# Kernel tuning notes

Hardware: AMD Instinct MI355X
Metric: run time of the kernel (lower is better)

## Reference

```python
import jax, jax.numpy as jnp
import numpy as np

ROPE_BASE = 10000.0

def _rope(x):
    # x: (B, T, H, hd); rotate-half RoPE
    B, T, H, hd = x.shape
    half = hd // 2
    inv_freq = 1.0 / (ROPE_BASE ** (jnp.arange(half, dtype=jnp.float32) / half))
    ang = jnp.arange(T, dtype=jnp.float32)[:, None] * inv_freq[None, :]  # (T, half)
    cos = jnp.cos(ang)[None, :, None, :]
    sin = jnp.sin(ang)[None, :, None, :]
    x1, x2 = x[..., :half], x[..., half:]
    return jnp.concatenate([x1 * cos - x2 * sin, x1 * sin + x2 * cos], axis=-1)

def setup_inputs() -> dict:
    key = jax.random.key(0)
    k1, k2, k3 = jax.random.split(key, 3)
    B, T, D = 4, 2048, 2048
    x = jax.random.normal(k1, (B, T, D), dtype=jnp.float32)
    attn_mask = jnp.ones((B, T), dtype=bool)
    w_qkv = jax.random.normal(k2, (3 * D, D), dtype=jnp.float32) * (D ** -0.5)
    w_out = jax.random.normal(k3, (D, D), dtype=jnp.float32) * (D ** -0.5)
    return {"x": x, "attn_mask": attn_mask, "is_causal": 1, "w_qkv": w_qkv, "w_out": w_out}

def reference(x, attn_mask, is_causal, w_qkv, w_out):
    B, T, D = x.shape
    H = 16
    hd = D // H
    qkv = jnp.einsum('btd,ed->bte', x, w_qkv)  # (B, T, 3D)
    q, k, v = jnp.split(qkv, 3, axis=2)
    q = _rope(q.reshape(B, T, H, hd))
    k = _rope(k.reshape(B, T, H, hd))
    v = v.reshape(B, T, H, hd)
    scale = 1.0 / jnp.sqrt(jnp.float32(hd))
    scores = jnp.einsum('bqhd,bkhd->bhqk', q, k) * scale  # (B, H, T, T)
    if is_causal:
        mask = jnp.tril(jnp.ones((T, T), dtype=bool))[None, None]
    else:
        mask = attn_mask[:, None, None, :]  # (B,1,1,T)
    scores = jnp.where(mask, scores, jnp.finfo(scores.dtype).min)
    attn = jax.nn.softmax(scores, axis=-1)
    y = jnp.einsum('bhqk,bkhd->bqhd', attn, v).reshape(B, T, D)
    return jnp.einsum('btd,ed->bte', y, w_out)
```

## Files before the change

kernel.cpp:

```cpp
#include <hip/hip_runtime.h>
#include <stdint.h>
#include <stddef.h>

typedef float f32x4 __attribute__((ext_vector_type(4)));
typedef __bf16 bf16x8 __attribute__((ext_vector_type(8)));
typedef short s16x4 __attribute__((ext_vector_type(4)));

#define DEVI static __device__ __forceinline__

DEVI float bf2f(unsigned short u) {
  unsigned int x = ((unsigned int)u) << 16;
  float f;
  __builtin_memcpy(&f, &x, 4);
  return f;
}
DEVI unsigned short f2bf(float f) {
  unsigned int x;
  __builtin_memcpy(&x, &f, 4);
  unsigned int r = (x + 0x7fffu + ((x >> 16) & 1u)) >> 16;
  return (unsigned short)r;
}

DEVI void async16(const void* g, void* l) {
  __builtin_amdgcn_global_load_lds((__attribute__((address_space(1))) void*)g,
                                   (__attribute__((address_space(3))) void*)l,
                                   16, 0, 0);
}

#define BAR_LGKM()                                          \
  do {                                                      \
    asm volatile("s_waitcnt lgkmcnt(0)" ::: "memory");      \
    __builtin_amdgcn_s_barrier();                           \
    __builtin_amdgcn_sched_barrier(0);                      \
  } while (0)

#define BAR_VM(N)                                               \
  do {                                                          \
    asm volatile("s_waitcnt vmcnt(" #N ")" ::: "memory");       \
    __builtin_amdgcn_s_barrier();                               \
    __builtin_amdgcn_sched_barrier(0);                          \
  } while (0)

__global__ __launch_bounds__(256) void cvt_bf16(const float* __restrict__ in,
                                                unsigned short* __restrict__ out, int n) {
  int i = (blockIdx.x * 256 + threadIdx.x) * 4;
  if (i >= n) return;
  float4 v = *(const float4*)(in + i);
  s16x4 o;
  o[0] = (short)f2bf(v.x);
  o[1] = (short)f2bf(v.y);
  o[2] = (short)f2bf(v.z);
  o[3] = (short)f2bf(v.w);
  *(s16x4*)(out + i) = o;
}

__global__ __launch_bounds__(256) void rope_table(float* __restrict__ tab) {
  int idx = blockIdx.x * 256 + threadIdx.x;
  if (idx >= 2048 * 64) return;
  int tt = idx >> 6, j = idx & 63;
  float inv = powf(10000.0f, -(float)j * (1.0f / 64.0f));
  float ang = (float)tt * inv;
  tab[tt * 128 + j] = cosf(ang);
  tab[tt * 128 + 64 + j] = sinf(ang);
}

__global__ __launch_bounds__(256) void rope_apply(unsigned short* __restrict__ Qg,
                                                  unsigned short* __restrict__ Kg,
                                                  const float* __restrict__ tab) {
  const float S2 = 0.0883883476483184f * 1.44269504088896341f;
  int idx = blockIdx.x * 256 + threadIdx.x;
  int j4 = idx & 15;
  int tt = (idx >> 4) & 2047;
  int bh = idx >> 15;
  size_t base = ((size_t)bh * 2048 + tt) * 128;
  f32x4 c4 = *(const f32x4*)(tab + tt * 128 + j4 * 4);
  f32x4 s4 = *(const f32x4*)(tab + tt * 128 + 64 + j4 * 4);
  s16x4 q1 = *(const s16x4*)(Qg + base + j4 * 4);
  s16x4 q2 = *(const s16x4*)(Qg + base + 64 + j4 * 4);
  s16x4 k1 = *(const s16x4*)(Kg + base + j4 * 4);
  s16x4 k2 = *(const s16x4*)(Kg + base + 64 + j4 * 4);
  s16x4 o1, o2, p1, p2;
#pragma unroll
  for (int r = 0; r < 4; ++r) {
    float c = c4[r], s = s4[r];
    float a = bf2f((unsigned short)q1[r]), b2 = bf2f((unsigned short)q2[r]);
    o1[r] = (short)f2bf((a * c - b2 * s) * S2);
    o2[r] = (short)f2bf((a * s + b2 * c) * S2);
    float ka = bf2f((unsigned short)k1[r]), kb = bf2f((unsigned short)k2[r]);
    p1[r] = (short)f2bf(ka * c - kb * s);
    p2[r] = (short)f2bf(ka * s + kb * c);
  }
  *(s16x4*)(Qg + base + j4 * 4) = o1;
  *(s16x4*)(Qg + base + 64 + j4 * 4) = o2;
  *(s16x4*)(Kg + base + j4 * 4) = p1;
  *(s16x4*)(Kg + base + 64 + j4 * 4) = p2;
}

template <int EPI>
__global__ __launch_bounds__(512) void gemm256(const unsigned short* __restrict__ A,
                                               const unsigned short* __restrict__ B,
                                               float* __restrict__ C, int M, int N, int K,
                                               unsigned short* __restrict__ Q,
                                               unsigned short* __restrict__ Kk,
                                               unsigned short* __restrict__ VT) {
  __shared__ __attribute__((aligned(128))) unsigned short Al[2][2][8192];
  __shared__ __attribute__((aligned(128))) unsigned short Bl[2][2][8192];
  const int t = threadIdx.x;
  const int lane = t & 63;
  const int w = t >> 6, wr = w >> 2, wc = w & 3;
  const int g = lane >> 4, lr = lane & 15;

  const int id = blockIdx.y * gridDim.x + blockIdx.x;
  const int nwg = gridDim.x * gridDim.y;
  const int wg = (id & 7) * (nwg >> 3) + (id >> 3);
  const int bm = (wg / gridDim.x) * 256, bn = (wg % gridDim.x) * 256;

  const unsigned short* aptr = A + (size_t)bm * K;
  const unsigned short* bptr = B + (size_t)bn * K;

  const int srow = t >> 3;
  const int sslot = (t & 7) ^ (srow & 7);

#define STG(arr, mat, p, h, kt)                                                   \
  do {                                                                            \
    const unsigned short* _s =                                                    \
        (mat) + (size_t)((h) * 128 + srow) * K + (size_t)(kt) * 64 + sslot * 8;   \
    async16(_s, &arr[p][h][t * 8]);                                               \
    async16(_s + (size_t)64 * K, &arr[p][h][t * 8 + 4096]);                       \
  } while (0)

  const int u0 = ((g ^ (lr & 7)) * 8) + lr * 64;
  const int u1 = (((4 + g) ^ (lr & 7)) * 8) + lr * 64;

#define LDA_(p, mh)                                                               \
  _Pragma("unroll") for (int mf = 0; mf < 4; ++mf) {                              \
    af[mf][0] = *(const bf16x8*)&Al[p][wr][(mh) * 4096 + mf * 1024 + u0];         \
    af[mf][1] = *(const bf16x8*)&Al[p][wr][(mh) * 4096 + mf * 1024 + u1];         \
  }
#define LDB_(dst, p, nh)                                                          \
  _Pragma("unroll") for (int nf = 0; nf < 2; ++nf) {                              \
    dst[nf][0] = *(const bf16x8*)&Bl[p][wc >> 1][(wc & 1) * 4096 + (nh) * 2048 +  \
                                                 nf * 1024 + u0];                 \
    dst[nf][1] = *(const bf16x8*)&Bl[p][wc >> 1][(wc & 1) * 4096 + (nh) * 2048 +  \
                                                 nf * 1024 + u1];                 \
  }
#define MMA_(bsrc, mh, nh)                                                        \
  __builtin_amdgcn_s_setprio(1);                                                  \
  _Pragma("unroll") for (int mf = 0; mf < 4; ++mf)                                \
      _Pragma("unroll") for (int nf = 0; nf < 2; ++nf) {                          \
    acc[(mh) * 4 + mf][(nh) * 2 + nf] = __builtin_amdgcn_mfma_f32_16x16x32_bf16(  \
        af[mf][0], bsrc[nf][0], acc[(mh) * 4 + mf][(nh) * 2 + nf], 0, 0, 0);      \
    acc[(mh) * 4 + mf][(nh) * 2 + nf] = __builtin_amdgcn_mfma_f32_16x16x32_bf16(  \
        af[mf][1], bsrc[nf][1], acc[(mh) * 4 + mf][(nh) * 2 + nf], 0, 0, 0);      \
  }                                                                               \
  __builtin_amdgcn_s_setprio(0);
#define BARR() __builtin_amdgcn_s_barrier();

  f32x4 acc[8][4] = {};
  bf16x8 af[4][2], bfrA[2][2], bfrB[2][2];

  STG(Al, aptr, 0, 0, 0);
  STG(Al, aptr, 0, 1, 0);
  STG(Bl, bptr, 0, 0, 0);
  STG(Bl, bptr, 0, 1, 0);
  STG(Bl, bptr, 1, 0, 1);
  STG(Bl, bptr, 1, 1, 1);
  asm volatile("s_waitcnt vmcnt(4)" ::: "memory");
  __builtin_amdgcn_s_barrier();

  const int NITER = K >> 7;
  for (int i = 0; i < NITER; ++i) {
    const bool G = (i + 1 < NITER);
    const int t1 = 2 * i + 1, t2 = 2 * i + 2, t3 = 2 * i + 3;

    LDA_(0, 0);
    LDB_(bfrA, 0, 0);
    STG(Al, aptr, 1, 0, t1);
    STG(Al, aptr, 1, 1, t1);
    BARR();
    MMA_(bfrA, 0, 0);
    BARR();
    LDB_(bfrB, 0, 1);
    BARR();
    MMA_(bfrB, 0, 1);
    BARR();
    LDA_(0, 1);
    BARR();
    MMA_(bfrB, 1, 1);
    BARR();
    if (G) {
      STG(Bl, bptr, 0, 0, t2);
      asm volatile("s_waitcnt vmcnt(2)" ::: "memory");
    } else {
      asm volatile("s_waitcnt vmcnt(0)" ::: "memory");
    }
    BARR();
    MMA_(bfrA, 1, 0);
    BARR();
    LDA_(1, 0);
    LDB_(bfrA, 1, 0);
    if (G) STG(Bl, bptr, 0, 1, t2);
    BARR();
    MMA_(bfrA, 0, 0);
    BARR();
    LDB_(bfrB, 1, 1);
    if (G) STG(Al, aptr, 0, 0, t2);
    BARR();
    MMA_(bfrB, 0, 1);
    BARR();
    LDA_(1, 1);
    if (G) STG(Al, aptr, 0, 1, t2);
    BARR();
    MMA_(bfrB, 1, 1);
    BARR();
    if (G) {
      STG(Bl, bptr, 1, 0, t3);
      STG(Bl, bptr, 1, 1, t3);
      asm volatile("s_waitcnt vmcnt(4)" ::: "memory");
    }
    BARR();
    MMA_(bfrA, 1, 0);
    BARR();
  }
#undef STG
#undef LDA_
#undef LDB_
#undef MMA_
#undef BARR

  if (EPI == 0) {
#pragma unroll
    for (int mp = 0; mp < 8; ++mp) {
      int m0 = bm + wr * 128 + (mp >> 2) * 64 + (mp & 3) * 16 + g * 4;
#pragma unroll
      for (int nfi = 0; nfi < 4; ++nfi) {
        int n = bn + wc * 64 + (nfi >> 1) * 32 + (nfi & 1) * 16 + lr;
#pragma unroll
        for (int r = 0; r < 4; ++r) C[(size_t)(m0 + r) * N + n] = acc[mp][nfi][r];
      }
    }
  } else {
    const int bi = bm >> 11;
    const int tbase = bm & 2047;
#pragma unroll
    for (int nfi = 0; nfi < 4; ++nfi) {
      int e = bn + wc * 64 + (nfi >> 1) * 32 + (nfi & 1) * 16 + lr;
      int region = e >> 11;
      int e2 = e & 2047;
      int h = e2 >> 7, d = e2 & 127;
      int bh = bi * 16 + h;
#pragma unroll
      for (int mp = 0; mp < 8; ++mp) {
        int trow = tbase + wr * 128 + (mp >> 2) * 64 + (mp & 3) * 16 + g * 4;
        if (region == 2) {
          s16x4 pk;
#pragma unroll
          for (int r = 0; r < 4; ++r) pk[r] = (short)f2bf(acc[mp][nfi][r]);
          *(s16x4*)(VT + ((size_t)bh * 128 + d) * 2048 + trow) = pk;
        } else {
          unsigned short* dst = (region == 0) ? Q : Kk;
#pragma unroll
          for (int r = 0; r < 4; ++r)
            dst[((size_t)bh * 2048 + trow + r) * 128 + d] = f2bf(acc[mp][nfi][r]);
        }
      }
    }
  }
}

__global__ __launch_bounds__(256) void flash_attn(const unsigned short* __restrict__ Qg,
                                                  const unsigned short* __restrict__ Kg,
                                                  const unsigned short* __restrict__ VTg,
                                                  unsigned short* __restrict__ Yg,
                                                  const int* __restrict__ iscausal,
                                                  const unsigned char* __restrict__ amask) {
  __shared__ __attribute__((aligned(128))) unsigned short Ks[2][64 * 128];
  __shared__ __attribute__((aligned(128))) unsigned short Vs[2][128 * 64];
  __shared__ __attribute__((aligned(128))) unsigned short Ps[4][16 * 72];

  const int t = threadIdx.x, lane = t & 63, w = t >> 6;
  const int g = lane >> 4, lr = lane & 15;
  const int id = blockIdx.x;
  const int xcd = id & 7, j5 = id >> 3;
  const int bh = xcd * 8 + (j5 >> 5);
  const int qbi = 31 - (j5 & 31);
  const int b = bh >> 4;
  const int qb = qbi * 64;
  const int causal = iscausal[0] != 0;
  const int nt = causal ? (qbi + 1) : 32;

  const unsigned short* qrow = Qg + ((size_t)bh * 2048 + qb + w * 16 + lr) * 128;
  bf16x8 qf[4];
#pragma unroll
  for (int ds = 0; ds < 4; ++ds) qf[ds] = *(const bf16x8*)(qrow + ds * 32 + g * 8);

  const unsigned short* Kbase = Kg + (size_t)bh * 2048 * 128;
  const unsigned short* Vbase = VTg + (size_t)bh * 128 * 2048;

  const int rK = t >> 4, sK = ((t & 15) ^ rK);
  const int rV = t >> 3, sV = ((t & 7) ^ ((t >> 3) & 7));

#define STAGE(KT, P)                                                                    \
  do {                                                                                  \
    const int _kv = (KT) * 64;                                                          \
    _Pragma("unroll") for (int c = 0; c < 4; ++c)                                       \
        async16(Kbase + (size_t)(_kv + c * 16 + rK) * 128 + sK * 8,                     \
                &Ks[P][c * 2048 + t * 8]);                                              \
    _Pragma("unroll") for (int c = 0; c < 4; ++c)                                       \
        async16(Vbase + (size_t)(c * 32 + rV) * 2048 + _kv + sV * 8,                    \
                &Vs[P][c * 2048 + t * 8]);                                              \
  } while (0)

  unsigned int oi[4] = {0x3F803F80u, 0x3F803F80u, 0x3F803F80u, 0x3F803F80u};
  bf16x8 ones;
  __builtin_memcpy(&ones, oi, 16);

  f32x4 acc[8] = {};
  f32x4 accl = {0.f, 0.f, 0.f, 0.f};
  float mrow[4] = {-1e30f, -1e30f, -1e30f, -1e30f};

  STAGE(0, 0);

  for (int kt = 0; kt < nt; ++kt) {
    const int p = kt & 1;
    const int kv0 = kt * 64;
    if (kt + 1 < nt) {
      STAGE(kt + 1, p ^ 1);
      BAR_VM(8);
    } else {
      BAR_VM(0);
    }

    f32x4 s[4] = {};
    __builtin_amdgcn_s_setprio(1);
#pragma unroll
    for (int cf = 0; cf < 4; ++cf)
#pragma unroll
      for (int ds = 0; ds < 4; ++ds) {
        bf16x8 kf = *(const bf16x8*)(&Ks[p][(cf * 16 + lr) * 128 + (((ds * 4 + g) ^ lr) * 8)]);
        s[cf] = __builtin_amdgcn_mfma_f32_16x16x32_bf16(qf[ds], kf, s[cf], 0, 0, 0);
      }
    __builtin_amdgcn_s_setprio(0);

    const int q0 = qb + w * 16 + g * 4;
    if (causal) {
      if (kt == qbi) {
#pragma unroll
        for (int cf = 0; cf < 4; ++cf) {
          int kvg = kv0 + cf * 16 + lr;
#pragma unroll
          for (int r = 0; r < 4; ++r)
            if (kvg > q0 + r) s[cf][r] = -1e30f;
        }
      }
    } else {
#pragma unroll
      for (int cf = 0; cf < 4; ++cf) {
        int kvg = kv0 + cf * 16 + lr;
        if (!amask[(size_t)b * 2048 + kvg]) {
#pragma unroll
          for (int r = 0; r < 4; ++r) s[cf][r] = -1e30f;
        }
      }
    }

    f32x4 lm;
#pragma unroll
    for (int r = 0; r < 4; ++r)
      lm[r] = fmaxf(fmaxf(s[0][r], s[1][r]), fmaxf(s[2][r], s[3][r]));
    bool ok = true;
#pragma unroll
    for (int r = 0; r < 4; ++r) ok = ok && (lm[r] <= mrow[r] + 8.0f);
    if (!__all(ok)) {
      f32x4 mx = lm;
#pragma unroll
      for (int off = 8; off >= 1; off >>= 1)
#pragma unroll
        for (int r = 0; r < 4; ++r) mx[r] = fmaxf(mx[r], __shfl_xor(mx[r], off));
#pragma unroll
      for (int r = 0; r < 4; ++r) {
        float mn = fmaxf(mrow[r], mx[r]);
        float corr = exp2f(mrow[r] - mn);
        mrow[r] = mn;
        accl[r] *= corr;
#pragma unroll
        for (int jf = 0; jf < 8; ++jf) acc[jf][r] *= corr;
      }
    }

#pragma unroll
    for (int cf = 0; cf < 4; ++cf)
#pragma unroll
      for (int r = 0; r < 4; ++r) s[cf][r] = exp2f(s[cf][r] - mrow[r]);

    unsigned short* Pw = &Ps[w][0];
#pragma unroll
    for (int cf = 0; cf < 4; ++cf)
#pragma unroll
      for (int r = 0; r < 4; ++r) Pw[(g * 4 + r) * 72 + cf * 16 + lr] = f2bf(s[cf][r]);
    asm volatile("s_waitcnt lgkmcnt(0)" ::: "memory");
    __builtin_amdgcn_sched_barrier(0);

    bf16x8 pa0 = *(const bf16x8*)(Pw + lr * 72 + g * 8);
    bf16x8 pa1 = *(const bf16x8*)(Pw + lr * 72 + 32 + g * 8);

    accl = __builtin_amdgcn_mfma_f32_16x16x32_bf16(pa0, ones, accl, 0, 0, 0);
    accl = __builtin_amdgcn_mfma_f32_16x16x32_bf16(pa1, ones, accl, 0, 0, 0);

    __builtin_amdgcn_s_setprio(1);
#pragma unroll
    for (int jf = 0; jf < 8; ++jf) {
      bf16x8 v0 = *(const bf16x8*)(&Vs[p][(jf * 16 + lr) * 64 + ((g ^ (lr & 7)) * 8)]);
      bf16x8 v1 = *(const bf16x8*)(&Vs[p][(jf * 16 + lr) * 64 + (((4 + g) ^ (lr & 7)) * 8)]);
      acc[jf] = __builtin_amdgcn_mfma_f32_16x16x32_bf16(pa0, v0, acc[jf], 0, 0, 0);
      acc[jf] = __builtin_amdgcn_mfma_f32_16x16x32_bf16(pa1, v1, acc[jf], 0, 0, 0);
    }
    __builtin_amdgcn_s_setprio(0);

    BAR_LGKM();
  }
#undef STAGE

  const int h = bh & 15;
  float rl[4];
#pragma unroll
  for (int r = 0; r < 4; ++r) rl[r] = __builtin_amdgcn_rcpf(accl[r]);
#pragma unroll
  for (int jf = 0; jf < 8; ++jf)
#pragma unroll
    for (int r = 0; r < 4; ++r) {
      int tt = qb + w * 16 + g * 4 + r;
      Yg[((size_t)b * 2048 + tt) * 2048 + h * 128 + jf * 16 + lr] = f2bf(acc[jf][r] * rl[r]);
    }
}

extern "C" void kernel_launch(void* const* d_in, const int* in_sizes, int n_in, void* d_out,
                              int out_size, void* d_ws, size_t ws_size, hipStream_t stream) {
  const float* x = (const float*)d_in[0];
  const unsigned char* amask = (const unsigned char*)d_in[1];
  const int* iscausal = (const int*)d_in[2];
  const float* wqkv = (const float*)d_in[3];
  const float* wout = (const float*)d_in[4];
  float* out = (float*)d_out;

  const size_t MT = 8192, D = 2048, ND = 6144;
  unsigned short* xb = (unsigned short*)d_ws;
  unsigned short* wqkvb = xb + MT * D;
  unsigned short* woutb = wqkvb + ND * D;
  unsigned short* q = woutb + D * D;
  unsigned short* k = q + MT * D;
  unsigned short* vt = k + MT * D;
  unsigned short* y = vt + MT * D;
  float* tab = (float*)(y + MT * D);
  if (ws_size < (size_t)(100663296) * 2 + 2048 * 128 * 4) return;

  cvt_bf16<<<dim3(16384), dim3(256), 0, stream>>>(x, xb, (int)(MT * D));
  cvt_bf16<<<dim3(12288), dim3(256), 0, stream>>>(wqkv, wqkvb, (int)(ND * D));
  cvt_bf16<<<dim3(4096), dim3(256), 0, stream>>>(wout, woutb, (int)(D * D));
  rope_table<<<dim3(512), dim3(256), 0, stream>>>(tab);
  gemm256<1><<<dim3(24, 32), dim3(512), 0, stream>>>(xb, wqkvb, nullptr, 8192, 6144, 2048, q, k, vt);
  rope_apply<<<dim3(8192), dim3(256), 0, stream>>>(q, k, tab);
  flash_attn<<<dim3(2048), dim3(256), 0, stream>>>(q, k, vt, y, iscausal, amask);
  gemm256<0><<<dim3(8, 32), dim3(512), 0, stream>>>(y, woutb, out, 8192, 2048, 2048, nullptr,
                                                    nullptr, nullptr);
}
```

Measured before the change: 485.0 us.

## Restructure GEMM main loop into four larger MFMA phases with fewer barriers

Each k-tile now loads the full B fragment (four n-subtiles) at once and issues larger MFMA groups per A half. The schedule drops from eight compute phases to four per iteration, which halves the barrier count. Global-to-LDS staging is regrouped with adjusted vmcnt waits, and the epilogue column mapping is changed to match the new fragment order. In exchange there is more register pressure from the larger B fragment and a different overlap between loads and compute.

```diff
diff --git a/kernel.cpp b/kernel.cpp
--- a/kernel.cpp
+++ b/kernel.cpp
@@ -137,27 +137,25 @@
     af[mf][0] = *(const bf16x8*)&Al[p][wr][(mh) * 4096 + mf * 1024 + u0];         \
     af[mf][1] = *(const bf16x8*)&Al[p][wr][(mh) * 4096 + mf * 1024 + u1];         \
   }
-#define LDB_(dst, p, nh)                                                          \
-  _Pragma("unroll") for (int nf = 0; nf < 2; ++nf) {                              \
-    dst[nf][0] = *(const bf16x8*)&Bl[p][wc >> 1][(wc & 1) * 4096 + (nh) * 2048 +  \
-                                                 nf * 1024 + u0];                 \
-    dst[nf][1] = *(const bf16x8*)&Bl[p][wc >> 1][(wc & 1) * 4096 + (nh) * 2048 +  \
-                                                 nf * 1024 + u1];                 \
-  }
-#define MMA_(bsrc, mh, nh)                                                        \
+#define LDB_(p)                                                                   \
+  _Pragma("unroll") for (int nf = 0; nf < 4; ++nf) {                              \
+    bfr[nf][0] = *(const bf16x8*)&Bl[p][wc >> 1][(wc & 1) * 4096 + nf * 1024 + u0]; \
+    bfr[nf][1] = *(const bf16x8*)&Bl[p][wc >> 1][(wc & 1) * 4096 + nf * 1024 + u1]; \
+  }
+#define MMA_(mh)                                                                  \
   __builtin_amdgcn_s_setprio(1);                                                  \
   _Pragma("unroll") for (int mf = 0; mf < 4; ++mf)                                \
-      _Pragma("unroll") for (int nf = 0; nf < 2; ++nf) {                          \
-    acc[(mh) * 4 + mf][(nh) * 2 + nf] = __builtin_amdgcn_mfma_f32_16x16x32_bf16(  \
-        af[mf][0], bsrc[nf][0], acc[(mh) * 4 + mf][(nh) * 2 + nf], 0, 0, 0);      \
-    acc[(mh) * 4 + mf][(nh) * 2 + nf] = __builtin_amdgcn_mfma_f32_16x16x32_bf16(  \
-        af[mf][1], bsrc[nf][1], acc[(mh) * 4 + mf][(nh) * 2 + nf], 0, 0, 0);      \
+      _Pragma("unroll") for (int nf = 0; nf < 4; ++nf) {                          \
+    acc[(mh) * 4 + mf][nf] = __builtin_amdgcn_mfma_f32_16x16x32_bf16(             \
+        af[mf][0], bfr[nf][0], acc[(mh) * 4 + mf][nf], 0, 0, 0);                  \
+    acc[(mh) * 4 + mf][nf] = __builtin_amdgcn_mfma_f32_16x16x32_bf16(             \
+        af[mf][1], bfr[nf][1], acc[(mh) * 4 + mf][nf], 0, 0, 0);                  \
   }                                                                               \
   __builtin_amdgcn_s_setprio(0);
 #define BARR() __builtin_amdgcn_s_barrier();
 
   f32x4 acc[8][4] = {};
-  bf16x8 af[4][2], bfrA[2][2], bfrB[2][2];
+  bf16x8 af[4][2], bfr[4][2];
 
   STG(Al, aptr, 0, 0, 0);
   STG(Al, aptr, 0, 1, 0);
@@ -165,7 +163,8 @@
   STG(Bl, bptr, 0, 1, 0);
   STG(Bl, bptr, 1, 0, 1);
   STG(Bl, bptr, 1, 1, 1);
-  asm volatile("s_waitcnt vmcnt(4)" ::: "memory");
+  STG(Al, aptr, 1, 0, 1);
+  asm volatile("s_waitcnt vmcnt(6)" ::: "memory");
   __builtin_amdgcn_s_barrier();
 
   const int NITER = K >> 7;
@@ -174,52 +173,43 @@
     const int t1 = 2 * i + 1, t2 = 2 * i + 2, t3 = 2 * i + 3;
 
     LDA_(0, 0);
-    LDB_(bfrA, 0, 0);
-    STG(Al, aptr, 1, 0, t1);
+    LDB_(0);
     STG(Al, aptr, 1, 1, t1);
     BARR();
-    MMA_(bfrA, 0, 0);
-    BARR();
-    LDB_(bfrB, 0, 1);
-    BARR();
-    MMA_(bfrB, 0, 1);
+    MMA_(0);
     BARR();
     LDA_(0, 1);
-    BARR();
-    MMA_(bfrB, 1, 1);
-    BARR();
     if (G) {
       STG(Bl, bptr, 0, 0, t2);
+      STG(Bl, bptr, 0, 1, t2);
+      STG(Al, aptr, 0, 0, t2);
+      asm volatile("s_waitcnt vmcnt(8)" ::: "memory");
+    } else {
       asm volatile("s_waitcnt vmcnt(2)" ::: "memory");
+    }
+    BARR();
+    MMA_(1);
+    BARR();
+    LDA_(1, 0);
+    LDB_(1);
+    if (G) {
+      STG(Al, aptr, 0, 1, t2);
+      asm volatile("s_waitcnt vmcnt(8)" ::: "memory");
     } else {
       asm volatile("s_waitcnt vmcnt(0)" ::: "memory");
     }
     BARR();
-    MMA_(bfrA, 1, 0);
-    BARR();
-    LDA_(1, 0);
-    LDB_(bfrA, 1, 0);
-    if (G) STG(Bl, bptr, 0, 1, t2);
-    BARR();
-    MMA_(bfrA, 0, 0);
-    BARR();
-    LDB_(bfrB, 1, 1);
-    if (G) STG(Al, aptr, 0, 0, t2);
-    BARR();
-    MMA_(bfrB, 0, 1);
+    MMA_(0);
     BARR();
     LDA_(1, 1);
-    if (G) STG(Al, aptr, 0, 1, t2);
-    BARR();
-    MMA_(bfrB, 1, 1);
-    BARR();
     if (G) {
       STG(Bl, bptr, 1, 0, t3);
       STG(Bl, bptr, 1, 1, t3);
-      asm volatile("s_waitcnt vmcnt(4)" ::: "memory");
-    }
-    BARR();
-    MMA_(bfrA, 1, 0);
+      STG(Al, aptr, 1, 0, t3);
+      asm volatile("s_waitcnt vmcnt(6)" ::: "memory");
+    }
+    BARR();
+    MMA_(1);
     BARR();
   }
 #undef STG
@@ -233,18 +223,18 @@
     for (int mp = 0; mp < 8; ++mp) {
       int m0 = bm + wr * 128 + (mp >> 2) * 64 + (mp & 3) * 16 + g * 4;
 #pragma unroll
-      for (int nfi = 0; nfi < 4; ++nfi) {
-        int n = bn + wc * 64 + (nfi >> 1) * 32 + (nfi & 1) * 16 + lr;
-#pragma unroll
-        for (int r = 0; r < 4; ++r) C[(size_t)(m0 + r) * N + n] = acc[mp][nfi][r];
+      for (int nf = 0; nf < 4; ++nf) {
+        int n = bn + wc * 64 + nf * 16 + lr;
+#pragma unroll
+        for (int r = 0; r < 4; ++r) C[(size_t)(m0 + r) * N + n] = acc[mp][nf][r];
       }
     }
   } else {
     const int bi = bm >> 11;
     const int tbase = bm & 2047;
 #pragma unroll
-    for (int nfi = 0; nfi < 4; ++nfi) {
-      int e = bn + wc * 64 + (nfi >> 1) * 32 + (nfi & 1) * 16 + lr;
+    for (int nf = 0; nf < 4; ++nf) {
+      int e = bn + wc * 64 + nf * 16 + lr;
       int region = e >> 11;
       int e2 = e & 2047;
       int h = e2 >> 7, d = e2 & 127;
@@ -255,13 +245,13 @@
         if (region == 2) {
           s16x4 pk;
 #pragma unroll
-          for (int r = 0; r < 4; ++r) pk[r] = (short)f2bf(acc[mp][nfi][r]);
+          for (int r = 0; r < 4; ++r) pk[r] = (short)f2bf(acc[mp][nf][r]);
           *(s16x4*)(VT + ((size_t)bh * 128 + d) * 2048 + trow) = pk;
         } else {
           unsigned short* dst = (region == 0) ? Q : Kk;
 #pragma unroll
           for (int r = 0; r < 4; ++r)
-            dst[((size_t)bh * 2048 + trow + r) * 128 + d] = f2bf(acc[mp][nfi][r]);
+            dst[((size_t)bh * 2048 + trow + r) * 128 + d] = f2bf(acc[mp][nf][r]);
         }
       }
     }
```

Measured after the change: 489.4 us. About the same (+0.9%).

## Fuse RoPE and Q scaling into QKV GEMM epilogue via LDS partner exchange

Applied to the files above, without the earlier changes.

Removes the separate rope_apply pass over Q and K by applying the rotation in the QKV GEMM epilogue. The rotate-half partner values come from the neighbouring wave's accumulators, which are exchanged through a shared-memory buffer that reuses the GEMM staging space. The block-to-tile mapping is also reordered so consecutive workgroups walk along M instead of N. This saves one read and write of Q and K, at the cost of extra LDS traffic, syncs and scattered table loads in the epilogue.

```diff
diff --git a/kernel.cpp b/kernel.cpp
--- a/kernel.cpp
+++ b/kernel.cpp
@@ -64,47 +64,15 @@
   tab[tt * 128 + 64 + j] = sinf(ang);
 }
 
-__global__ __launch_bounds__(256) void rope_apply(unsigned short* __restrict__ Qg,
-                                                  unsigned short* __restrict__ Kg,
-                                                  const float* __restrict__ tab) {
-  const float S2 = 0.0883883476483184f * 1.44269504088896341f;
-  int idx = blockIdx.x * 256 + threadIdx.x;
-  int j4 = idx & 15;
-  int tt = (idx >> 4) & 2047;
-  int bh = idx >> 15;
-  size_t base = ((size_t)bh * 2048 + tt) * 128;
-  f32x4 c4 = *(const f32x4*)(tab + tt * 128 + j4 * 4);
-  f32x4 s4 = *(const f32x4*)(tab + tt * 128 + 64 + j4 * 4);
-  s16x4 q1 = *(const s16x4*)(Qg + base + j4 * 4);
-  s16x4 q2 = *(const s16x4*)(Qg + base + 64 + j4 * 4);
-  s16x4 k1 = *(const s16x4*)(Kg + base + j4 * 4);
-  s16x4 k2 = *(const s16x4*)(Kg + base + 64 + j4 * 4);
-  s16x4 o1, o2, p1, p2;
-#pragma unroll
-  for (int r = 0; r < 4; ++r) {
-    float c = c4[r], s = s4[r];
-    float a = bf2f((unsigned short)q1[r]), b2 = bf2f((unsigned short)q2[r]);
-    o1[r] = (short)f2bf((a * c - b2 * s) * S2);
-    o2[r] = (short)f2bf((a * s + b2 * c) * S2);
-    float ka = bf2f((unsigned short)k1[r]), kb = bf2f((unsigned short)k2[r]);
-    p1[r] = (short)f2bf(ka * c - kb * s);
-    p2[r] = (short)f2bf(ka * s + kb * c);
-  }
-  *(s16x4*)(Qg + base + j4 * 4) = o1;
-  *(s16x4*)(Qg + base + 64 + j4 * 4) = o2;
-  *(s16x4*)(Kg + base + j4 * 4) = p1;
-  *(s16x4*)(Kg + base + 64 + j4 * 4) = p2;
-}
-
 template <int EPI>
 __global__ __launch_bounds__(512) void gemm256(const unsigned short* __restrict__ A,
                                                const unsigned short* __restrict__ B,
                                                float* __restrict__ C, int M, int N, int K,
                                                unsigned short* __restrict__ Q,
                                                unsigned short* __restrict__ Kk,
-                                               unsigned short* __restrict__ VT) {
-  __shared__ __attribute__((aligned(128))) unsigned short Al[2][2][8192];
-  __shared__ __attribute__((aligned(128))) unsigned short Bl[2][2][8192];
+                                               unsigned short* __restrict__ VT,
+                                               const float* __restrict__ tab) {
+  __shared__ __attribute__((aligned(128))) unsigned short SH[65536];
   const int t = threadIdx.x;
   const int lane = t & 63;
   const int w = t >> 6, wr = w >> 2, wc = w & 3;
@@ -113,7 +81,8 @@
   const int id = blockIdx.y * gridDim.x + blockIdx.x;
   const int nwg = gridDim.x * gridDim.y;
   const int wg = (id & 7) * (nwg >> 3) + (id >> 3);
-  const int bm = (wg / gridDim.x) * 256, bn = (wg % gridDim.x) * 256;
+  const int mt = M >> 8;
+  const int bm = (wg % mt) * 256, bn = (wg / mt) * 256;
 
   const unsigned short* aptr = A + (size_t)bm * K;
   const unsigned short* bptr = B + (size_t)bn * K;
@@ -121,12 +90,15 @@
   const int srow = t >> 3;
   const int sslot = (t & 7) ^ (srow & 7);
 
-#define STG(arr, mat, p, h, kt)                                                   \
+#define SHA(p, h) (SH + (p) * 16384 + (h) * 8192)
+#define SHB(p, h) (SH + 32768 + (p) * 16384 + (h) * 8192)
+
+#define STG(dstp, mat, h, kt)                                                     \
   do {                                                                            \
     const unsigned short* _s =                                                    \
         (mat) + (size_t)((h) * 128 + srow) * K + (size_t)(kt) * 64 + sslot * 8;   \
-    async16(_s, &arr[p][h][t * 8]);                                               \
-    async16(_s + (size_t)64 * K, &arr[p][h][t * 8 + 4096]);                       \
+    async16(_s, (dstp) + t * 8);                                                  \
+    async16(_s + (size_t)64 * K, (dstp) + t * 8 + 4096);                          \
   } while (0)
 
   const int u0 = ((g ^ (lr & 7)) * 8) + lr * 64;
@@ -134,15 +106,15 @@
 
 #define LDA_(p, mh)                                                               \
   _Pragma("unroll") for (int mf = 0; mf < 4; ++mf) {                              \
-    af[mf][0] = *(const bf16x8*)&Al[p][wr][(mh) * 4096 + mf * 1024 + u0];         \
-    af[mf][1] = *(const bf16x8*)&Al[p][wr][(mh) * 4096 + mf * 1024 + u1];         \
+    af[mf][0] = *(const bf16x8*)(SHA(p, wr) + (mh) * 4096 + mf * 1024 + u0);      \
+    af[mf][1] = *(const bf16x8*)(SHA(p, wr) + (mh) * 4096 + mf * 1024 + u1);      \
   }
 #define LDB_(dst, p, nh)                                                          \
   _Pragma("unroll") for (int nf = 0; nf < 2; ++nf) {                              \
-    dst[nf][0] = *(const bf16x8*)&Bl[p][wc >> 1][(wc & 1) * 4096 + (nh) * 2048 +  \
-                                                 nf * 1024 + u0];                 \
-    dst[nf][1] = *(const bf16x8*)&Bl[p][wc >> 1][(wc & 1) * 4096 + (nh) * 2048 +  \
-                                                 nf * 1024 + u1];                 \
+    dst[nf][0] = *(const bf16x8*)(SHB(p, wc >> 1) + (wc & 1) * 4096 +             \
+                                  (nh) * 2048 + nf * 1024 + u0);                  \
+    dst[nf][1] = *(const bf16x8*)(SHB(p, wc >> 1) + (wc & 1) * 4096 +             \
+                                  (nh) * 2048 + nf * 1024 + u1);                  \
   }
 #define MMA_(bsrc, mh, nh)                                                        \
   __builtin_amdgcn_s_setprio(1);                                                  \
@@ -159,12 +131,12 @@
   f32x4 acc[8][4] = {};
   bf16x8 af[4][2], bfrA[2][2], bfrB[2][2];
 
-  STG(Al, aptr, 0, 0, 0);
-  STG(Al, aptr, 0, 1, 0);
-  STG(Bl, bptr, 0, 0, 0);
-  STG(Bl, bptr, 0, 1, 0);
-  STG(Bl, bptr, 1, 0, 1);
-  STG(Bl, bptr, 1, 1, 1);
+  STG(SHA(0, 0), aptr, 0, 0);
+  STG(SHA(0, 1), aptr, 1, 0);
+  STG(SHB(0, 0), bptr, 0, 0);
+  STG(SHB(0, 1), bptr, 1, 0);
+  STG(SHB(1, 0), bptr, 0, 1);
+  STG(SHB(1, 1), bptr, 1, 1);
   asm volatile("s_waitcnt vmcnt(4)" ::: "memory");
   __builtin_amdgcn_s_barrier();
 
@@ -175,8 +147,8 @@
 
     LDA_(0, 0);
     LDB_(bfrA, 0, 0);
-    STG(Al, aptr, 1, 0, t1);
-    STG(Al, aptr, 1, 1, t1);
+    STG(SHA(1, 0), aptr, 0, t1);
+    STG(SHA(1, 1), aptr, 1, t1);
     BARR();
     MMA_(bfrA, 0, 0);
     BARR();
@@ -189,7 +161,7 @@
     MMA_(bfrB, 1, 1);
     BARR();
     if (G) {
-      STG(Bl, bptr, 0, 0, t2);
+      STG(SHB(0, 0), bptr, 0, t2);
       asm volatile("s_waitcnt vmcnt(2)" ::: "memory");
     } else {
       asm volatile("s_waitcnt vmcnt(0)" ::: "memory");
@@ -199,23 +171,23 @@
     BARR();
     LDA_(1, 0);
     LDB_(bfrA, 1, 0);
-    if (G) STG(Bl, bptr, 0, 1, t2);
+    if (G) STG(SHB(0, 1), bptr, 1, t2);
     BARR();
     MMA_(bfrA, 0, 0);
     BARR();
     LDB_(bfrB, 1, 1);
-    if (G) STG(Al, aptr, 0, 0, t2);
+    if (G) STG(SHA(0, 0), aptr, 0, t2);
     BARR();
     MMA_(bfrB, 0, 1);
     BARR();
     LDA_(1, 1);
-    if (G) STG(Al, aptr, 0, 1, t2);
+    if (G) STG(SHA(0, 1), aptr, 1, t2);
     BARR();
     MMA_(bfrB, 1, 1);
     BARR();
     if (G) {
-      STG(Bl, bptr, 1, 0, t3);
-      STG(Bl, bptr, 1, 1, t3);
+      STG(SHB(1, 0), bptr, 0, t3);
+      STG(SHB(1, 1), bptr, 1, t3);
       asm volatile("s_waitcnt vmcnt(4)" ::: "memory");
     }
     BARR();
@@ -242,30 +214,62 @@
   } else {
     const int bi = bm >> 11;
     const int tbase = bm & 2047;
-#pragma unroll
-    for (int nfi = 0; nfi < 4; ++nfi) {
-      int e = bn + wc * 64 + (nfi >> 1) * 32 + (nfi & 1) * 16 + lr;
-      int region = e >> 11;
-      int e2 = e & 2047;
-      int h = e2 >> 7, d = e2 & 127;
-      int bh = bi * 16 + h;
-#pragma unroll
-      for (int mp = 0; mp < 8; ++mp) {
-        int trow = tbase + wr * 128 + (mp >> 2) * 64 + (mp & 3) * 16 + g * 4;
-        if (region == 2) {
+    const int region = bn >> 11;
+    if (region == 2) {
+#pragma unroll
+      for (int nfi = 0; nfi < 4; ++nfi) {
+        int e2 = (bn & 2047) + wc * 64 + (nfi >> 1) * 32 + (nfi & 1) * 16 + lr;
+        int h = e2 >> 7, d = e2 & 127;
+        int bh = bi * 16 + h;
+#pragma unroll
+        for (int mp = 0; mp < 8; ++mp) {
+          int trow = tbase + wr * 128 + (mp >> 2) * 64 + (mp & 3) * 16 + g * 4;
           s16x4 pk;
 #pragma unroll
           for (int r = 0; r < 4; ++r) pk[r] = (short)f2bf(acc[mp][nfi][r]);
           *(s16x4*)(VT + ((size_t)bh * 128 + d) * 2048 + trow) = pk;
-        } else {
-          unsigned short* dst = (region == 0) ? Q : Kk;
+        }
+      }
+    } else {
+      unsigned short* dst = (region == 0) ? Q : Kk;
+      const float scq = (region == 0) ? (0.0883883476483184f * 1.44269504088896341f) : 1.0f;
+      __syncthreads();
+      unsigned short* myb = SH + w * 8192;
+#pragma unroll
+      for (int mp = 0; mp < 8; ++mp)
+#pragma unroll
+        for (int nfi = 0; nfi < 4; ++nfi)
 #pragma unroll
           for (int r = 0; r < 4; ++r)
-            dst[((size_t)bh * 2048 + trow + r) * 128 + d] = f2bf(acc[mp][nfi][r]);
+            myb[mp * 1024 + nfi * 256 + r * 64 + g * 16 + lr] = f2bf(acc[mp][nfi][r]);
+      __syncthreads();
+      const unsigned short* pb = SH + (w ^ 1) * 8192;
+      const int odd = wc & 1;
+#pragma unroll
+      for (int nfi = 0; nfi < 4; ++nfi) {
+        int j = (nfi >> 1) * 32 + (nfi & 1) * 16 + lr;
+        int e2 = (bn & 2047) + wc * 64 + j - odd * 64 + odd * 64;
+        e2 = (bn & 2047) + wc * 64 + (nfi >> 1) * 32 + (nfi & 1) * 16 + lr;
+        int h = e2 >> 7, d = e2 & 127;
+        int bh = bi * 16 + h;
+#pragma unroll
+        for (int mp = 0; mp < 8; ++mp) {
+          int tt0 = tbase + wr * 128 + (mp >> 2) * 64 + (mp & 3) * 16 + g * 4;
+#pragma unroll
+          for (int r = 0; r < 4; ++r) {
+            float x1 = acc[mp][nfi][r];
+            float x2 = bf2f(pb[mp * 1024 + nfi * 256 + r * 64 + g * 16 + lr]);
+            const float* tr = tab + (size_t)(tt0 + r) * 128 + j;
+            float cv = tr[0], sv = tr[64];
+            float o = odd ? (x2 * sv + x1 * cv) : (x1 * cv - x2 * sv);
+            dst[((size_t)bh * 2048 + tt0 + r) * 128 + d] = f2bf(o * scq);
+          }
         }
       }
     }
   }
+#undef SHA
+#undef SHB
 }
 
 __global__ __launch_bounds__(256) void flash_attn(const unsigned short* __restrict__ Qg,
@@ -458,9 +462,9 @@
   cvt_bf16<<<dim3(12288), dim3(256), 0, stream>>>(wqkv, wqkvb, (int)(ND * D));
   cvt_bf16<<<dim3(4096), dim3(256), 0, stream>>>(wout, woutb, (int)(D * D));
   rope_table<<<dim3(512), dim3(256), 0, stream>>>(tab);
-  gemm256<1><<<dim3(24, 32), dim3(512), 0, stream>>>(xb, wqkvb, nullptr, 8192, 6144, 2048, q, k, vt);
-  rope_apply<<<dim3(8192), dim3(256), 0, stream>>>(q, k, tab);
+  gemm256<1><<<dim3(24, 32), dim3(512), 0, stream>>>(xb, wqkvb, nullptr, 8192, 6144, 2048, q, k,
+                                                     vt, tab);
   flash_attn<<<dim3(2048), dim3(256), 0, stream>>>(q, k, vt, y, iscausal, amask);
   gemm256<0><<<dim3(8, 32), dim3(512), 0, stream>>>(y, woutb, out, 8192, 2048, 2048, nullptr,
-                                                    nullptr, nullptr);
-}
+                                                    nullptr, nullptr, nullptr);
+}
```

Result: slower. 566.9 us (+16.9%).
